# Optimization experiments

Hardware: AMD Instinct MI355X
Metric: run time of the kernel (lower is better)

## Reference

```python
import jax, jax.numpy as jnp
import numpy as np

H = 1024

def _lstm_layer(x, w_ih, w_hh, b):
    # x: [B, T, D] -> outputs [B, T, H], final (h, c) [B, H]
    B = x.shape[0]
    x_proj = jnp.einsum('btd,dg->btg', x, w_ih) + b  # [B, T, 4H]
    xp_t = jnp.swapaxes(x_proj, 0, 1)  # [T, B, 4H]

    def step(carry, xt):
        h, c = carry
        gates = xt + h @ w_hh  # [B, 4H]
        i = jax.nn.sigmoid(gates[:, :H])
        f = jax.nn.sigmoid(gates[:, H:2 * H])
        g = jnp.tanh(gates[:, 2 * H:3 * H])
        o = jax.nn.sigmoid(gates[:, 3 * H:])
        c = f * c + i * g
        h = o * jnp.tanh(c)
        return (h, c), h

    init = (jnp.zeros((B, H), x.dtype), jnp.zeros((B, H), x.dtype))
    (h_n, c_n), ys = jax.lax.scan(step, init, xp_t)
    return jnp.swapaxes(ys, 0, 1), h_n, c_n


def setup_inputs() -> dict:
    key = jax.random.key(0)
    ks = jax.random.split(key, 5)
    s = 0.1
    b = jnp.zeros((4 * H,), jnp.float32).at[H:2 * H].set(1.0)
    return {
        'x': jax.random.normal(ks[0], (32, 512, 1024), jnp.float32),
        'w_ih0': jax.random.uniform(ks[1], (1024, 4 * H), jnp.float32, -s, s),
        'w_hh0': jax.random.uniform(ks[2], (H, 4 * H), jnp.float32, -s, s),
        'b0': b,
        'w_ih1': jax.random.uniform(ks[3], (H, 4 * H), jnp.float32, -s, s),
        'w_hh1': jax.random.uniform(ks[4], (H, 4 * H), jnp.float32, -s, s),
        'b1': b,
    }


def reference(x, w_ih0, w_hh0, b0, w_ih1, w_hh1, b1):
    # Eval mode: LockedDropout / DropConnect are identity.
    y0, h0, c0 = _lstm_layer(x, w_ih0, w_hh0, b0)
    y1, h1, c1 = _lstm_layer(y0, w_ih1, w_hh1, b1)
    h_n = jnp.stack([h0, h1], axis=0)
    c_n = jnp.stack([c0, c1], axis=0)
    return y1, h_n, c_n
```

## Files before the change

kernel.cpp:

```cpp
#include <hip/hip_runtime.h>
#include <hip/hip_bf16.h>


constexpr int Hh = 1024;
constexpr int Bb = 32;
constexpr int Tt = 512;
constexpr int NWG = 256;
constexpr int NUG = 128;
constexpr int PLE  = 32 * 1024;
constexpr int ST3E = 3 * PLE;

typedef float f32x4 __attribute__((ext_vector_type(4)));
typedef int   i32x4 __attribute__((ext_vector_type(4)));

__device__ inline void mfma_bf16(f32x4& acc, i32x4 a, i32x4 b) {
    asm("s_nop 2\n\tv_mfma_f32_16x16x32_bf16 %0, %1, %2, %0"
        : "+v"(acc) : "v"(a), "v"(b));
}

__device__ inline i32x4 uload_x4(const void* p) {
    i32x4 r;
    asm volatile("global_load_dwordx4 %0, %1, off sc0 sc1\n\ts_waitcnt vmcnt(0)"
                 : "=&v"(r) : "v"(p) : "memory");
    return r;
}
__device__ inline void ustore_x4(void* p, i32x4 v) {
    asm volatile("global_store_dwordx4 %0, %1, off sc0 sc1"
                 :: "v"(p), "v"(v) : "memory");
}
__device__ inline i32x4 pload_x4(const unsigned short* p) {
    return *(const i32x4*)p;
}
__device__ inline void astore_u32(unsigned int* p, unsigned v) {
    __hip_atomic_store(p, v, __ATOMIC_RELAXED, __HIP_MEMORY_SCOPE_AGENT);
}
__device__ inline unsigned aload_u32(const unsigned int* p) {
    return __hip_atomic_load(p, __ATOMIC_RELAXED, __HIP_MEMORY_SCOPE_AGENT);
}

__device__ inline unsigned short f2bf(float f) {
    unsigned u = __float_as_uint(f);
    u += 0x7fffu + ((u >> 16) & 1u);
    return (unsigned short)(u >> 16);
}
__device__ inline float bf2f(unsigned short s) {
    return __uint_as_float((unsigned)s << 16);
}

__device__ inline float sigm(float x)  { return 1.f / (1.f + __expf(-x)); }
__device__ inline float tanh_f(float x){ return 1.f - 2.f / (__expf(2.f * x) + 1.f); }

__global__ __launch_bounds__(256) void k_xT(const float* __restrict__ x,
                                            unsigned short* __restrict__ xh,
                                            unsigned short* __restrict__ xl,
                                            int use_lo) {
    int bid = blockIdx.x;
    int t = bid >> 5, b = bid & 31;
    size_t o = ((size_t)t * Bb + b) * Hh;
    if (t == Tt) {
        ushort4 z = {0, 0, 0, 0};
        ((ushort4*)(xh + o))[threadIdx.x] = z;
        if (use_lo) ((ushort4*)(xl + o))[threadIdx.x] = z;
        return;
    }
    const float4* src = (const float4*)(x + ((size_t)b * Tt + t) * Hh);
    float4 v = src[threadIdx.x];
    ushort4 hi;
    hi.x = f2bf(v.x); hi.y = f2bf(v.y); hi.z = f2bf(v.z); hi.w = f2bf(v.w);
    ((ushort4*)(xh + o))[threadIdx.x] = hi;
    if (use_lo) {
        ushort4 lo;
        lo.x = f2bf(v.x - bf2f(hi.x));
        lo.y = f2bf(v.y - bf2f(hi.y));
        lo.z = f2bf(v.z - bf2f(hi.z));
        lo.w = f2bf(v.w - bf2f(hi.w));
        ((ushort4*)(xl + o))[threadIdx.x] = lo;
    }
}

__global__ __launch_bounds__(256) void k_warr(const float* __restrict__ w0,
                                              const float* __restrict__ w1,
                                              const float* __restrict__ w2,
                                              const float* __restrict__ w3,
                                              unsigned short* __restrict__ wh,
                                              unsigned short* __restrict__ wl,
                                              int use_lo) {
    int bid = blockIdx.x;
    int mat = bid >> 7, ug = bid & 127;
    const float* W = (mat == 0) ? w0 : (mat == 1) ? w1 : (mat == 2) ? w2 : w3;
    size_t dbase = ((size_t)(mat * NUG + ug) * 32) * Hh;
    size_t dlo   = ((size_t)(((mat >> 1) & 1) * NUG + ug) * 32) * Hh;
    const bool want_lo = use_lo && ((mat & 1) == 0);
    for (int it = 0; it < 128; ++it) {
        int idx = it * 256 + (int)threadIdx.x;
        int col = idx >> 10, k = idx & 1023;
        int cg = (col >> 3) * Hh + ug * 8 + (col & 7);
        float w = W[(size_t)k * 4096 + cg];
        unsigned short hi = f2bf(w);
        wh[dbase + (size_t)col * Hh + k] = hi;
        if (want_lo) wl[dlo + (size_t)col * Hh + k] = f2bf(w - bf2f(hi));
    }
}

template <bool USE_LO>
__global__ __launch_bounds__(512, 2) void k_lstm(
    const unsigned short* __restrict__ xTh,
    const unsigned short* __restrict__ xTl,
    const unsigned short* __restrict__ warrh,
    const unsigned short* __restrict__ warrl,
    unsigned int* __restrict__ hp0,
    unsigned int* __restrict__ hp1,
    unsigned int* __restrict__ flags,
    unsigned int* __restrict__ ectr,
    unsigned int* __restrict__ dflags,
    unsigned int* __restrict__ pfl,
    float*        __restrict__ pex,
    unsigned short* __restrict__ hstage,
    const float* __restrict__ b0,
    const float* __restrict__ b1,
    float* __restrict__ out)
{
    __shared__ float red[2][8][32][33];
    __shared__ float psum[2][32][33];
    __shared__ unsigned hsh[2][32][4];
    __shared__ int sRank;

    const int tid  = threadIdx.x;
    const int wave = tid >> 6;
    const int l    = tid & 63;
    const int wg   = blockIdx.x;
    const int kh   = wg & 1;
    const int ug   = wg >> 1;
    const int pwg  = wg ^ 1;

    unsigned xraw;
    asm volatile("s_getreg_b32 %0, hwreg(20, 0, 32)" : "=s"(xraw));
    const int xcd = (int)(xraw & 7u);
    if (tid == 0) sRank = (int)atomicAdd(&ectr[(size_t)xcd * 32], 1u);
    __syncthreads();
    const int rank = sRank;

    const int kbase = kh * 512 + ((wave + wg) & 7) * 64;

    i32x4 Bih0h[2][2], Bhh0h[2][2], Bih1h[2][2], Bhh1h[2][2];
    i32x4 Bih0l[2][2], Bih1l[2][2];
    {
        const size_t matStride = (size_t)NUG * 32 * Hh;
        const size_t wgOff = (size_t)ug * 32 * Hh;
        #pragma unroll
        for (int ch = 0; ch < 2; ++ch) {
            #pragma unroll
            for (int kk = 0; kk < 2; ++kk) {
                size_t off = (size_t)(ch * 16 + (l & 15)) * Hh
                             + kbase + kk * 32 + ((l >> 4) * 8);
                Bih0h[ch][kk] = pload_x4(warrh + 0 * matStride + wgOff + off);
                Bhh0h[ch][kk] = pload_x4(warrh + 1 * matStride + wgOff + off);
                Bih1h[ch][kk] = pload_x4(warrh + 2 * matStride + wgOff + off);
                Bhh1h[ch][kk] = pload_x4(warrh + 3 * matStride + wgOff + off);
                if (USE_LO) {
                    Bih0l[ch][kk] = pload_x4(warrl + 0 * matStride + wgOff + off);
                    Bih1l[ch][kk] = pload_x4(warrl + 1 * matStride + wgOff + off);
                }
            }
        }
        #pragma unroll
        for (int ch = 0; ch < 2; ++ch) {
            #pragma unroll
            for (int kk = 0; kk < 2; ++kk) {
                asm volatile("" : "+v"(Bih0h[ch][kk]), "+v"(Bhh0h[ch][kk]),
                                 "+v"(Bih1h[ch][kk]), "+v"(Bhh1h[ch][kk]));
                if (USE_LO)
                    asm volatile("" : "+v"(Bih0l[ch][kk]), "+v"(Bih1l[ch][kk]));
            }
        }
    }

    const int cid = tid & 127;
    const int cb  = cid & 31;
    const int ca  = (cid >> 5) & 3;
    const int a8  = kh * 4 + ca;
    const int cu  = wg * 4 + ca;
    const float* bias = (tid < 128) ? b0 : b1;
    const float bi  = bias[cu];
    const float bf_ = bias[Hh + cu];
    const float bg  = bias[2 * Hh + cu];
    const float bo  = bias[3 * Hh + cu];
    float c = 0.f;

    const int laneR = (l & 15);
    const int laneK = (l >> 4) * 8;

    f32x4 A0[2][2], A1[2][2];

    auto xterms = [&](int sidx) {
        const unsigned short* xh = xTh + (size_t)sidx * (Bb * Hh);
        const unsigned short* xl = xTl + (size_t)sidx * (Bb * Hh);
        #pragma unroll
        for (int m = 0; m < 2; ++m) {
            #pragma unroll
            for (int kk = 0; kk < 2; ++kk) {
                const size_t off = (size_t)(m * 16 + laneR) * Hh + kbase + kk * 32 + laneK;
                i32x4 axh = pload_x4(xh + off);
                i32x4 axl;
                if (USE_LO) axl = pload_x4(xl + off);
                #pragma unroll
                for (int ch = 0; ch < 2; ++ch) {
                    mfma_bf16(A0[m][ch], axh, Bih0h[ch][kk]);
                    if (USE_LO) {
                        mfma_bf16(A0[m][ch], axh, Bih0l[ch][kk]);
                        mfma_bf16(A0[m][ch], axl, Bih0h[ch][kk]);
                    }
                }
            }
        }
    };

    #pragma unroll
    for (int m = 0; m < 2; ++m)
        #pragma unroll
        for (int ch = 0; ch < 2; ++ch) A0[m][ch] = f32x4{0,0,0,0};
    xterms(0);

    unsigned nx = 0, nx32 = 0;

    for (int s = 0; s <= Tt; ++s) {
        const int par_w = s & 1;
        const int par_r = par_w ^ 1;
        const size_t parWOff32 = (size_t)par_w * (Bb * Hh);
        const size_t parROff32 = (size_t)par_r * (Bb * Hh);
        const unsigned short* stb = hstage + ((size_t)(s & 1) * 8 + xcd) * ST3E;
        const unsigned tgt = (unsigned)(s + 1);

        #pragma unroll
        for (int m = 0; m < 2; ++m)
            #pragma unroll
            for (int ch = 0; ch < 2; ++ch) A1[m][ch] = f32x4{0,0,0,0};

        #pragma unroll
        for (int m = 0; m < 2; ++m) {
            i32x4 g0h[2], g1h[2], g0l[2];
            #pragma unroll
            for (int kk = 0; kk < 2; ++kk) {
                const size_t off = (size_t)(m * 16 + laneR) * Hh + kbase + kk * 32 + laneK;
                g0h[kk] = pload_x4(stb + off);
                g1h[kk] = pload_x4(stb + 2 * PLE + off);
                if (USE_LO)
                    g0l[kk] = pload_x4(stb + PLE + off);
            }
            #pragma unroll
            for (int ch = 0; ch < 2; ++ch) {
                #pragma unroll
                for (int kk = 0; kk < 2; ++kk) {
                    mfma_bf16(A0[m][ch], g0h[kk], Bhh0h[ch][kk]);
                    mfma_bf16(A1[m][ch], g0h[kk], Bih1h[ch][kk]);
                    mfma_bf16(A1[m][ch], g1h[kk], Bhh1h[ch][kk]);
                    if (USE_LO) {
                        mfma_bf16(A0[m][ch], g0l[kk], Bhh0h[ch][kk]);
                        mfma_bf16(A1[m][ch], g0h[kk], Bih1l[ch][kk]);
                        mfma_bf16(A1[m][ch], g0l[kk], Bih1h[ch][kk]);
                    }
                }
            }
        }
        asm("s_nop 7\n\ts_nop 7"
            : "+v"(A0[0][0]), "+v"(A0[0][1]), "+v"(A0[1][0]), "+v"(A0[1][1]),
              "+v"(A1[0][0]), "+v"(A1[0][1]), "+v"(A1[1][0]), "+v"(A1[1][1]));

        {
            const int r0 = (l >> 4) * 4;
            const int cc = l & 15;
            #pragma unroll
            for (int m = 0; m < 2; ++m)
                #pragma unroll
                for (int ch = 0; ch < 2; ++ch)
                    #pragma unroll
                    for (int r = 0; r < 4; ++r) {
                        red[0][wave][m * 16 + r0 + r][ch * 16 + cc] = A0[m][ch][r];
                        red[1][wave][m * 16 + r0 + r][ch * 16 + cc] = A1[m][ch][r];
                    }
        }
        __syncthreads();

        {
            const int ly = tid >> 8, u = tid & 255;
            const int rr = u >> 3, c4 = (u & 7) * 4;
            float p0 = 0, p1 = 0, p2 = 0, p3 = 0;
            #pragma unroll
            for (int w = 0; w < 8; ++w) {
                p0 += red[ly][w][rr][c4];
                p1 += red[ly][w][rr][c4 + 1];
                p2 += red[ly][w][rr][c4 + 2];
                p3 += red[ly][w][rr][c4 + 3];
            }
            psum[ly][rr][c4] = p0;  psum[ly][rr][c4 + 1] = p1;
            psum[ly][rr][c4 + 2] = p2; psum[ly][rr][c4 + 3] = p3;
        }
        __syncthreads();

        {
            if (tid < 256) {
                const int ly = tid >> 7, u = tid & 127;
                const int rr = u >> 2, q = u & 3;
                const int pc = q * 8 + (kh ^ 1) * 4;
                i32x4 hv;
                hv[0] = __float_as_int(psum[ly][rr][pc]);
                hv[1] = __float_as_int(psum[ly][rr][pc + 1]);
                hv[2] = __float_as_int(psum[ly][rr][pc + 2]);
                hv[3] = __float_as_int(psum[ly][rr][pc + 3]);
                ustore_x4(pex + (size_t)wg * 1024 + ((ly * 32 + rr) * 4 + q) * 4, hv);
            }
            asm volatile("s_waitcnt vmcnt(0)" ::: "memory");
            __syncthreads();
            if (tid == 0) astore_u32(pfl + (size_t)wg * 32, tgt);
            if (tid == 0) {
                while (aload_u32(pfl + (size_t)pwg * 32) < tgt)
                    __builtin_amdgcn_s_sleep(1);
            }
            __syncthreads();
            if (tid < 256) {
                const int ly = tid >> 7, u = tid & 127;
                const int rr = u >> 2, q = u & 3;
                const int mc = q * 8 + kh * 4;
                i32x4 v = uload_x4(pex + (size_t)pwg * 1024 + ((ly * 32 + rr) * 4 + q) * 4);
                psum[ly][rr][mc]     += __int_as_float(v[0]);
                psum[ly][rr][mc + 1] += __int_as_float(v[1]);
                psum[ly][rr][mc + 2] += __int_as_float(v[2]);
                psum[ly][rr][mc + 3] += __int_as_float(v[3]);
            }
            __syncthreads();
        }

        if (tid < 128) {
            if (s < Tt) {
                float vi = bi  + psum[0][cb][a8];
                float vf = bf_ + psum[0][cb][8 + a8];
                float vg = bg  + psum[0][cb][16 + a8];
                float vo = bo  + psum[0][cb][24 + a8];
                float ig = sigm(vi), fg = sigm(vf), gg = tanh_f(vg), og = sigm(vo);
                c = fg * c + ig * gg;
                float h = og * tanh_f(c);
                unsigned short hh = f2bf(h);
                unsigned short hl = f2bf(h - bf2f(hh));
                hsh[0][cb][ca] = (unsigned)hh | ((unsigned)hl << 16);
                if (s == Tt - 1) {
                    out[16777216 + cb * Hh + cu] = h;
                    out[16777216 + 65536 + cb * Hh + cu] = c;
                }
            }
        } else if (tid < 256) {
            if (s >= 1) {
                const int t = s - 1;
                float vi = bi  + psum[1][cb][a8];
                float vf = bf_ + psum[1][cb][8 + a8];
                float vg = bg  + psum[1][cb][16 + a8];
                float vo = bo  + psum[1][cb][24 + a8];
                float ig = sigm(vi), fg = sigm(vf), gg = tanh_f(vg), og = sigm(vo);
                c = fg * c + ig * gg;
                float h = og * tanh_f(c);
                unsigned short hh = f2bf(h);
                hsh[1][cb][ca] = (unsigned)hh;
                out[(size_t)cb * (Tt * Hh) + (size_t)t * Hh + cu] = h;
                if (s == Tt) {
                    out[16777216 + 32768 + cb * Hh + cu] = h;
                    out[16777216 + 65536 + 32768 + cb * Hh + cu] = c;
                }
            }
        }

        if (s < Tt) {
            __syncthreads();
            if (tid < 64) {
                const int buf = tid >> 5;
                const int cbb = tid & 31;
                if (buf == 0 || s >= 1) {
                    i32x4 hv;
                    hv[0] = (int)hsh[buf][cbb][0];
                    hv[1] = (int)hsh[buf][cbb][1];
                    hv[2] = (int)hsh[buf][cbb][2];
                    hv[3] = (int)hsh[buf][cbb][3];
                    unsigned int* dst = (buf ? (hp1 + parROff32) : (hp0 + parWOff32))
                                        + (size_t)cbb * Hh + wg * 4;
                    ustore_x4(dst, hv);
                }
            }
            asm volatile("s_waitcnt vmcnt(0)" ::: "memory");
            __syncthreads();
            if (tid == 0) astore_u32(flags + (size_t)wg * 32, tgt);

            #pragma unroll
            for (int m = 0; m < 2; ++m)
                #pragma unroll
                for (int ch = 0; ch < 2; ++ch) A0[m][ch] = f32x4{0,0,0,0};
            xterms(s + 1);

            int ok = 0;
            do {
                unsigned f = (tid < 256) ? aload_u32(flags + (size_t)tid * 32) : tgt;
                ok = __syncthreads_and((int)(f >= tgt));
                if (!ok) __builtin_amdgcn_s_sleep(2);
            } while (!ok);

            if (nx == 0) {
                nx = aload_u32(ectr + (size_t)xcd * 32);
                nx32 = nx < 32u ? nx : 32u;
            }

            unsigned short* dstb = hstage + ((size_t)((s + 1) & 1) * 8 + xcd) * ST3E;
            for (int r = rank; r < 32; r += (int)nx) {
                const int buf = r >> 4;
                const unsigned int* sp = (buf == 0) ? (hp0 + parWOff32)
                                                    : (hp1 + parROff32);
                const int e = (r & 15) * 2048 + tid * 4;
                i32x4 v = uload_x4(sp + e);
                ushort4 hi4;
                hi4.x = (unsigned short)((unsigned)v[0] & 0xffffu);
                hi4.y = (unsigned short)((unsigned)v[1] & 0xffffu);
                hi4.z = (unsigned short)((unsigned)v[2] & 0xffffu);
                hi4.w = (unsigned short)((unsigned)v[3] & 0xffffu);
                unsigned short* dh = dstb + (buf == 0 ? 0 : 2 * PLE) + e;
                *(ushort4*)dh = hi4;
                if (buf == 0) {
                    ushort4 lo4;
                    lo4.x = (unsigned short)((unsigned)v[0] >> 16);
                    lo4.y = (unsigned short)((unsigned)v[1] >> 16);
                    lo4.z = (unsigned short)((unsigned)v[2] >> 16);
                    lo4.w = (unsigned short)((unsigned)v[3] >> 16);
                    *(ushort4*)(dstb + PLE + e) = lo4;
                }
            }
            asm volatile("s_waitcnt vmcnt(0)" ::: "memory");
            __syncthreads();
            if (tid == 0 && rank < 32)
                astore_u32(dflags + ((size_t)xcd * 32 + rank) * 32, tgt);
            int ok2 = 0;
            do {
                unsigned f = (tid < (int)nx32)
                    ? aload_u32(dflags + ((size_t)xcd * 32 + tid) * 32) : tgt;
                ok2 = __syncthreads_and((int)(f >= tgt));
                if (!ok2) __builtin_amdgcn_s_sleep(2);
            } while (!ok2);
        }
    }
}

extern "C" void kernel_launch(void* const* d_in, const int* in_sizes, int n_in,
                              void* d_out, int out_size, void* d_ws, size_t ws_size,
                              hipStream_t stream) {
    const float* x     = (const float*)d_in[0];
    const float* w_ih0 = (const float*)d_in[1];
    const float* w_hh0 = (const float*)d_in[2];
    const float* b0    = (const float*)d_in[3];
    const float* w_ih1 = (const float*)d_in[4];
    const float* w_hh1 = (const float*)d_in[5];
    const float* b1    = (const float*)d_in[6];
    float* out = (float*)d_out;

    const size_t SZ_WARRH = 33554432;
    const size_t SZ_WARRL = 16777216;
    const size_t SZ_XT    = 33619968;
    const size_t SZ_HP    = 262144;
    const size_t SZ_FLAGS = 32768;
    const size_t SZ_ECTR  = 1024;
    const size_t SZ_DFLG  = 32768;
    const size_t SZ_PFL   = 32768;
    const size_t SZ_PEX   = 1048576;
    const size_t SZ_STAGE = 3145728;

    char* ws = (char*)d_ws;
    unsigned short* warrh = (unsigned short*)ws;
    unsigned short* warrl = (unsigned short*)(ws + SZ_WARRH);
    unsigned short* xTh   = (unsigned short*)(ws + SZ_WARRH + SZ_WARRL);
    unsigned short* xTl   = (unsigned short*)(ws + SZ_WARRH + SZ_WARRL + SZ_XT);
    char* zbase = ws + SZ_WARRH + SZ_WARRL + 2 * SZ_XT;
    unsigned int* hp0    = (unsigned int*)zbase;
    unsigned int* hp1    = (unsigned int*)(zbase + SZ_HP);
    unsigned int* flags  = (unsigned int*)(zbase + 2 * SZ_HP);
    unsigned int* ectr   = (unsigned int*)(zbase + 2 * SZ_HP + SZ_FLAGS);
    unsigned int* dflags = (unsigned int*)(zbase + 2 * SZ_HP + SZ_FLAGS + SZ_ECTR);
    unsigned int* pfl    = (unsigned int*)(zbase + 2 * SZ_HP + SZ_FLAGS + SZ_ECTR + SZ_DFLG);
    float*        pex    = (float*)(zbase + 2 * SZ_HP + SZ_FLAGS + SZ_ECTR + SZ_DFLG + SZ_PFL);
    unsigned short* hstage =
        (unsigned short*)(zbase + 2 * SZ_HP + SZ_FLAGS + SZ_ECTR + SZ_DFLG + SZ_PFL + SZ_PEX);

    const size_t ZSZ  = 2 * SZ_HP + SZ_FLAGS + SZ_ECTR + SZ_DFLG + SZ_PFL + SZ_PEX + SZ_STAGE;
    const size_t FULL = SZ_WARRH + SZ_WARRL + 2 * SZ_XT + ZSZ;
    const bool use_lo = ws_size >= FULL;

    hipMemsetAsync(zbase, 0, ZSZ, stream);
    hipLaunchKernelGGL(k_xT,   dim3(16416), dim3(256), 0, stream, x, xTh, xTl, (int)use_lo);
    hipLaunchKernelGGL(k_warr, dim3(512),   dim3(256), 0, stream,
                       w_ih0, w_hh0, w_ih1, w_hh1, warrh, warrl, (int)use_lo);
    if (use_lo) {
        hipLaunchKernelGGL(k_lstm<true>, dim3(256), dim3(512), 0, stream,
                           xTh, xTl, warrh, warrl, hp0, hp1,
                           flags, ectr, dflags, pfl, pex, hstage, b0, b1, out);
    } else {
        hipLaunchKernelGGL(k_lstm<false>, dim3(256), dim3(512), 0, stream,
                           xTh, xTl, warrh, warrl, hp0, hp1,
                           flags, ectr, dflags, pfl, pex, hstage, b0, b1, out);
    }
}
```

Measured before the change: 5.608 ms.

## Split K across four workgroups per 16-unit group instead of two

```diff
diff --git a/kernel.cpp b/kernel.cpp
--- a/kernel.cpp
+++ b/kernel.cpp
@@ -5,8 +5,7 @@
 constexpr int Hh = 1024;
 constexpr int Bb = 32;
 constexpr int Tt = 512;
-constexpr int NWG = 256;
-constexpr int NUG = 128;
+constexpr int NUG = 64;
 constexpr int PLE  = 32 * 1024;
 constexpr int ST3E = 3 * PLE;
 
@@ -86,15 +85,15 @@
                                               unsigned short* __restrict__ wl,
                                               int use_lo) {
     int bid = blockIdx.x;
-    int mat = bid >> 7, ug = bid & 127;
+    int mat = bid >> 6, ug = bid & 63;
     const float* W = (mat == 0) ? w0 : (mat == 1) ? w1 : (mat == 2) ? w2 : w3;
-    size_t dbase = ((size_t)(mat * NUG + ug) * 32) * Hh;
-    size_t dlo   = ((size_t)(((mat >> 1) & 1) * NUG + ug) * 32) * Hh;
+    size_t dbase = ((size_t)(mat * NUG + ug) * 64) * Hh;
+    size_t dlo   = ((size_t)(((mat >> 1) & 1) * NUG + ug) * 64) * Hh;
     const bool want_lo = use_lo && ((mat & 1) == 0);
-    for (int it = 0; it < 128; ++it) {
+    for (int it = 0; it < 256; ++it) {
         int idx = it * 256 + (int)threadIdx.x;
         int col = idx >> 10, k = idx & 1023;
-        int cg = (col >> 3) * Hh + ug * 8 + (col & 7);
+        int cg = (col >> 4) * Hh + ug * 16 + (col & 15);
         float w = W[(size_t)k * 4096 + cg];
         unsigned short hi = f2bf(w);
         wh[dbase + (size_t)col * Hh + k] = hi;
@@ -120,8 +119,8 @@
     const float* __restrict__ b1,
     float* __restrict__ out)
 {
-    __shared__ float red[2][8][32][33];
-    __shared__ float psum[2][32][33];
+    __shared__ float red[2][8][32][65];
+    __shared__ float psum[2][32][65];
     __shared__ unsigned hsh[2][32][4];
     __shared__ int sRank;
 
@@ -129,9 +128,9 @@
     const int wave = tid >> 6;
     const int l    = tid & 63;
     const int wg   = blockIdx.x;
-    const int kh   = wg & 1;
-    const int ug   = wg >> 1;
-    const int pwg  = wg ^ 1;
+    const int q    = wg & 3;
+    const int qb   = wg & ~3;
+    const int ug   = wg >> 2;
 
     unsigned xraw;
     asm volatile("s_getreg_b32 %0, hwreg(20, 0, 32)" : "=s"(xraw));
@@ -140,45 +139,38 @@
     __syncthreads();
     const int rank = sRank;
 
-    const int kbase = kh * 512 + ((wave + wg) & 7) * 64;
-
-    i32x4 Bih0h[2][2], Bhh0h[2][2], Bih1h[2][2], Bhh1h[2][2];
-    i32x4 Bih0l[2][2], Bih1l[2][2];
+    const int kbase = q * 256 + ((wave + wg) & 7) * 32;
+
+    i32x4 Bih0h[4], Bhh0h[4], Bih1h[4], Bhh1h[4];
+    i32x4 Bih0l[4], Bih1l[4];
     {
-        const size_t matStride = (size_t)NUG * 32 * Hh;
-        const size_t wgOff = (size_t)ug * 32 * Hh;
-        #pragma unroll
-        for (int ch = 0; ch < 2; ++ch) {
-            #pragma unroll
-            for (int kk = 0; kk < 2; ++kk) {
-                size_t off = (size_t)(ch * 16 + (l & 15)) * Hh
-                             + kbase + kk * 32 + ((l >> 4) * 8);
-                Bih0h[ch][kk] = pload_x4(warrh + 0 * matStride + wgOff + off);
-                Bhh0h[ch][kk] = pload_x4(warrh + 1 * matStride + wgOff + off);
-                Bih1h[ch][kk] = pload_x4(warrh + 2 * matStride + wgOff + off);
-                Bhh1h[ch][kk] = pload_x4(warrh + 3 * matStride + wgOff + off);
-                if (USE_LO) {
-                    Bih0l[ch][kk] = pload_x4(warrl + 0 * matStride + wgOff + off);
-                    Bih1l[ch][kk] = pload_x4(warrl + 1 * matStride + wgOff + off);
-                }
-            }
-        }
-        #pragma unroll
-        for (int ch = 0; ch < 2; ++ch) {
-            #pragma unroll
-            for (int kk = 0; kk < 2; ++kk) {
-                asm volatile("" : "+v"(Bih0h[ch][kk]), "+v"(Bhh0h[ch][kk]),
-                                 "+v"(Bih1h[ch][kk]), "+v"(Bhh1h[ch][kk]));
-                if (USE_LO)
-                    asm volatile("" : "+v"(Bih0l[ch][kk]), "+v"(Bih1l[ch][kk]));
-            }
+        const size_t matStride = (size_t)NUG * 64 * Hh;
+        const size_t wgOff = (size_t)ug * 64 * Hh;
+        #pragma unroll
+        for (int ch = 0; ch < 4; ++ch) {
+            size_t off = (size_t)(ch * 16 + (l & 15)) * Hh + kbase + ((l >> 4) * 8);
+            Bih0h[ch] = pload_x4(warrh + 0 * matStride + wgOff + off);
+            Bhh0h[ch] = pload_x4(warrh + 1 * matStride + wgOff + off);
+            Bih1h[ch] = pload_x4(warrh + 2 * matStride + wgOff + off);
+            Bhh1h[ch] = pload_x4(warrh + 3 * matStride + wgOff + off);
+            if (USE_LO) {
+                Bih0l[ch] = pload_x4(warrl + 0 * matStride + wgOff + off);
+                Bih1l[ch] = pload_x4(warrl + 1 * matStride + wgOff + off);
+            }
+        }
+        #pragma unroll
+        for (int ch = 0; ch < 4; ++ch) {
+            asm volatile("" : "+v"(Bih0h[ch]), "+v"(Bhh0h[ch]),
+                             "+v"(Bih1h[ch]), "+v"(Bhh1h[ch]));
+            if (USE_LO)
+                asm volatile("" : "+v"(Bih0l[ch]), "+v"(Bih1l[ch]));
         }
     }
 
     const int cid = tid & 127;
     const int cb  = cid & 31;
     const int ca  = (cid >> 5) & 3;
-    const int a8  = kh * 4 + ca;
+    const int a16 = q * 4 + ca;
     const int cu  = wg * 4 + ca;
     const float* bias = (tid < 128) ? b0 : b1;
     const float bi  = bias[cu];
@@ -190,26 +182,23 @@
     const int laneR = (l & 15);
     const int laneK = (l >> 4) * 8;
 
-    f32x4 A0[2][2], A1[2][2];
+    f32x4 A0[2][4], A1[2][4];
 
     auto xterms = [&](int sidx) {
         const unsigned short* xh = xTh + (size_t)sidx * (Bb * Hh);
         const unsigned short* xl = xTl + (size_t)sidx * (Bb * Hh);
         #pragma unroll
         for (int m = 0; m < 2; ++m) {
-            #pragma unroll
-            for (int kk = 0; kk < 2; ++kk) {
-                const size_t off = (size_t)(m * 16 + laneR) * Hh + kbase + kk * 32 + laneK;
-                i32x4 axh = pload_x4(xh + off);
-                i32x4 axl;
-                if (USE_LO) axl = pload_x4(xl + off);
-                #pragma unroll
-                for (int ch = 0; ch < 2; ++ch) {
-                    mfma_bf16(A0[m][ch], axh, Bih0h[ch][kk]);
-                    if (USE_LO) {
-                        mfma_bf16(A0[m][ch], axh, Bih0l[ch][kk]);
-                        mfma_bf16(A0[m][ch], axl, Bih0h[ch][kk]);
-                    }
+            const size_t off = (size_t)(m * 16 + laneR) * Hh + kbase + laneK;
+            i32x4 axh = pload_x4(xh + off);
+            i32x4 axl;
+            if (USE_LO) axl = pload_x4(xl + off);
+            #pragma unroll
+            for (int ch = 0; ch < 4; ++ch) {
+                mfma_bf16(A0[m][ch], axh, Bih0h[ch]);
+                if (USE_LO) {
+                    mfma_bf16(A0[m][ch], axh, Bih0l[ch]);
+                    mfma_bf16(A0[m][ch], axl, Bih0h[ch]);
                 }
             }
         }
@@ -218,7 +207,7 @@
     #pragma unroll
     for (int m = 0; m < 2; ++m)
         #pragma unroll
-        for (int ch = 0; ch < 2; ++ch) A0[m][ch] = f32x4{0,0,0,0};
+        for (int ch = 0; ch < 4; ++ch) A0[m][ch] = f32x4{0,0,0,0};
     xterms(0);
 
     unsigned nx = 0, nx32 = 0;
@@ -234,37 +223,32 @@
         #pragma unroll
         for (int m = 0; m < 2; ++m)
             #pragma unroll
-            for (int ch = 0; ch < 2; ++ch) A1[m][ch] = f32x4{0,0,0,0};
+            for (int ch = 0; ch < 4; ++ch) A1[m][ch] = f32x4{0,0,0,0};
 
         #pragma unroll
         for (int m = 0; m < 2; ++m) {
-            i32x4 g0h[2], g1h[2], g0l[2];
-            #pragma unroll
-            for (int kk = 0; kk < 2; ++kk) {
-                const size_t off = (size_t)(m * 16 + laneR) * Hh + kbase + kk * 32 + laneK;
-                g0h[kk] = pload_x4(stb + off);
-                g1h[kk] = pload_x4(stb + 2 * PLE + off);
-                if (USE_LO)
-                    g0l[kk] = pload_x4(stb + PLE + off);
-            }
-            #pragma unroll
-            for (int ch = 0; ch < 2; ++ch) {
-                #pragma unroll
-                for (int kk = 0; kk < 2; ++kk) {
-                    mfma_bf16(A0[m][ch], g0h[kk], Bhh0h[ch][kk]);
-                    mfma_bf16(A1[m][ch], g0h[kk], Bih1h[ch][kk]);
-                    mfma_bf16(A1[m][ch], g1h[kk], Bhh1h[ch][kk]);
-                    if (USE_LO) {
-                        mfma_bf16(A0[m][ch], g0l[kk], Bhh0h[ch][kk]);
-                        mfma_bf16(A1[m][ch], g0h[kk], Bih1l[ch][kk]);
-                        mfma_bf16(A1[m][ch], g0l[kk], Bih1h[ch][kk]);
-                    }
+            const size_t off = (size_t)(m * 16 + laneR) * Hh + kbase + laneK;
+            i32x4 g0h = pload_x4(stb + off);
+            i32x4 g1h = pload_x4(stb + 2 * PLE + off);
+            i32x4 g0l;
+            if (USE_LO) g0l = pload_x4(stb + PLE + off);
+            #pragma unroll
+            for (int ch = 0; ch < 4; ++ch) {
+                mfma_bf16(A0[m][ch], g0h, Bhh0h[ch]);
+                mfma_bf16(A1[m][ch], g0h, Bih1h[ch]);
+                mfma_bf16(A1[m][ch], g1h, Bhh1h[ch]);
+                if (USE_LO) {
+                    mfma_bf16(A0[m][ch], g0l, Bhh0h[ch]);
+                    mfma_bf16(A1[m][ch], g0h, Bih1l[ch]);
+                    mfma_bf16(A1[m][ch], g0l, Bih1h[ch]);
                 }
             }
         }
         asm("s_nop 7\n\ts_nop 7"
-            : "+v"(A0[0][0]), "+v"(A0[0][1]), "+v"(A0[1][0]), "+v"(A0[1][1]),
-              "+v"(A1[0][0]), "+v"(A1[0][1]), "+v"(A1[1][0]), "+v"(A1[1][1]));
+            : "+v"(A0[0][0]), "+v"(A0[0][1]), "+v"(A0[0][2]), "+v"(A0[0][3]),
+              "+v"(A0[1][0]), "+v"(A0[1][1]), "+v"(A0[1][2]), "+v"(A0[1][3]),
+              "+v"(A1[0][0]), "+v"(A1[0][1]), "+v"(A1[0][2]), "+v"(A1[0][3]),
+              "+v"(A1[1][0]), "+v"(A1[1][1]), "+v"(A1[1][2]), "+v"(A1[1][3]));
 
         {
             const int r0 = (l >> 4) * 4;
@@ -272,7 +256,7 @@
             #pragma unroll
             for (int m = 0; m < 2; ++m)
                 #pragma unroll
-                for (int ch = 0; ch < 2; ++ch)
+                for (int ch = 0; ch < 4; ++ch)
                     #pragma unroll
                     for (int r = 0; r < 4; ++r) {
                         red[0][wave][m * 16 + r0 + r][ch * 16 + cc] = A0[m][ch][r];
@@ -283,59 +267,69 @@
 
         {
             const int ly = tid >> 8, u = tid & 255;
-            const int rr = u >> 3, c4 = (u & 7) * 4;
-            float p0 = 0, p1 = 0, p2 = 0, p3 = 0;
-            #pragma unroll
-            for (int w = 0; w < 8; ++w) {
-                p0 += red[ly][w][rr][c4];
-                p1 += red[ly][w][rr][c4 + 1];
-                p2 += red[ly][w][rr][c4 + 2];
-                p3 += red[ly][w][rr][c4 + 3];
-            }
-            psum[ly][rr][c4] = p0;  psum[ly][rr][c4 + 1] = p1;
-            psum[ly][rr][c4 + 2] = p2; psum[ly][rr][c4 + 3] = p3;
+            const int rr = u >> 3, c8 = (u & 7) * 8;
+            float p[8];
+            #pragma unroll
+            for (int j = 0; j < 8; ++j) p[j] = 0.f;
+            #pragma unroll
+            for (int w = 0; w < 8; ++w)
+                #pragma unroll
+                for (int j = 0; j < 8; ++j) p[j] += red[ly][w][rr][c8 + j];
+            #pragma unroll
+            for (int j = 0; j < 8; ++j) psum[ly][rr][c8 + j] = p[j];
         }
         __syncthreads();
 
         {
-            if (tid < 256) {
-                const int ly = tid >> 7, u = tid & 127;
-                const int rr = u >> 2, q = u & 3;
-                const int pc = q * 8 + (kh ^ 1) * 4;
-                i32x4 hv;
-                hv[0] = __float_as_int(psum[ly][rr][pc]);
-                hv[1] = __float_as_int(psum[ly][rr][pc + 1]);
-                hv[2] = __float_as_int(psum[ly][rr][pc + 2]);
-                hv[3] = __float_as_int(psum[ly][rr][pc + 3]);
-                ustore_x4(pex + (size_t)wg * 1024 + ((ly * 32 + rr) * 4 + q) * 4, hv);
-            }
+            const int ly = tid >> 8, u = tid & 255;
+            const int rr = u >> 3, c8 = (u & 7) * 8;
+            float* base = pex + (size_t)wg * 4096 + ((size_t)ly * 32 + rr) * 64 + c8;
+            i32x4 v0, v1;
+            v0[0] = __float_as_int(psum[ly][rr][c8]);
+            v0[1] = __float_as_int(psum[ly][rr][c8 + 1]);
+            v0[2] = __float_as_int(psum[ly][rr][c8 + 2]);
+            v0[3] = __float_as_int(psum[ly][rr][c8 + 3]);
+            v1[0] = __float_as_int(psum[ly][rr][c8 + 4]);
+            v1[1] = __float_as_int(psum[ly][rr][c8 + 5]);
+            v1[2] = __float_as_int(psum[ly][rr][c8 + 6]);
+            v1[3] = __float_as_int(psum[ly][rr][c8 + 7]);
+            ustore_x4(base, v0);
+            ustore_x4(base + 4, v1);
             asm volatile("s_waitcnt vmcnt(0)" ::: "memory");
             __syncthreads();
             if (tid == 0) astore_u32(pfl + (size_t)wg * 32, tgt);
-            if (tid == 0) {
-                while (aload_u32(pfl + (size_t)pwg * 32) < tgt)
-                    __builtin_amdgcn_s_sleep(1);
-            }
-            __syncthreads();
+            int okp = 0;
+            do {
+                unsigned f = tgt;
+                if (tid < 4 && tid != q)
+                    f = aload_u32(pfl + (size_t)(qb + tid) * 32);
+                okp = __syncthreads_and((int)(f >= tgt));
+                if (!okp) __builtin_amdgcn_s_sleep(1);
+            } while (!okp);
             if (tid < 256) {
-                const int ly = tid >> 7, u = tid & 127;
-                const int rr = u >> 2, q = u & 3;
-                const int mc = q * 8 + kh * 4;
-                i32x4 v = uload_x4(pex + (size_t)pwg * 1024 + ((ly * 32 + rr) * 4 + q) * 4);
-                psum[ly][rr][mc]     += __int_as_float(v[0]);
-                psum[ly][rr][mc + 1] += __int_as_float(v[1]);
-                psum[ly][rr][mc + 2] += __int_as_float(v[2]);
-                psum[ly][rr][mc + 3] += __int_as_float(v[3]);
+                const int ly2 = tid >> 7, u2 = tid & 127;
+                const int rr2 = u2 >> 2, g = u2 & 3;
+                const int col = g * 16 + q * 4;
+                #pragma unroll
+                for (int pp = 0; pp < 4; ++pp) {
+                    if (pp == q) continue;
+                    i32x4 v = uload_x4(pex + (size_t)(qb + pp) * 4096
+                                       + ((size_t)ly2 * 32 + rr2) * 64 + col);
+                    psum[ly2][rr2][col]     += __int_as_float(v[0]);
+                    psum[ly2][rr2][col + 1] += __int_as_float(v[1]);
+                    psum[ly2][rr2][col + 2] += __int_as_float(v[2]);
+                    psum[ly2][rr2][col + 3] += __int_as_float(v[3]);
+                }
             }
             __syncthreads();
         }
 
         if (tid < 128) {
             if (s < Tt) {
-                float vi = bi  + psum[0][cb][a8];
-                float vf = bf_ + psum[0][cb][8 + a8];
-                float vg = bg  + psum[0][cb][16 + a8];
-                float vo = bo  + psum[0][cb][24 + a8];
+                float vi = bi  + psum[0][cb][a16];
+                float vf = bf_ + psum[0][cb][16 + a16];
+                float vg = bg  + psum[0][cb][32 + a16];
+                float vo = bo  + psum[0][cb][48 + a16];
                 float ig = sigm(vi), fg = sigm(vf), gg = tanh_f(vg), og = sigm(vo);
                 c = fg * c + ig * gg;
                 float h = og * tanh_f(c);
@@ -350,10 +344,10 @@
         } else if (tid < 256) {
             if (s >= 1) {
                 const int t = s - 1;
-                float vi = bi  + psum[1][cb][a8];
-                float vf = bf_ + psum[1][cb][8 + a8];
-                float vg = bg  + psum[1][cb][16 + a8];
-                float vo = bo  + psum[1][cb][24 + a8];
+                float vi = bi  + psum[1][cb][a16];
+                float vf = bf_ + psum[1][cb][16 + a16];
+                float vg = bg  + psum[1][cb][32 + a16];
+                float vo = bo  + psum[1][cb][48 + a16];
                 float ig = sigm(vi), fg = sigm(vf), gg = tanh_f(vg), og = sigm(vo);
                 c = fg * c + ig * gg;
                 float h = og * tanh_f(c);
@@ -390,7 +384,7 @@
             #pragma unroll
             for (int m = 0; m < 2; ++m)
                 #pragma unroll
-                for (int ch = 0; ch < 2; ++ch) A0[m][ch] = f32x4{0,0,0,0};
+                for (int ch = 0; ch < 4; ++ch) A0[m][ch] = f32x4{0,0,0,0};
             xterms(s + 1);
 
             int ok = 0;
@@ -463,7 +457,7 @@
     const size_t SZ_ECTR  = 1024;
     const size_t SZ_DFLG  = 32768;
     const size_t SZ_PFL   = 32768;
-    const size_t SZ_PEX   = 1048576;
+    const size_t SZ_PEX   = 4194304;
     const size_t SZ_STAGE = 3145728;
 
     char* ws = (char*)d_ws;
@@ -488,7 +482,7 @@
 
     hipMemsetAsync(zbase, 0, ZSZ, stream);
     hipLaunchKernelGGL(k_xT,   dim3(16416), dim3(256), 0, stream, x, xTh, xTl, (int)use_lo);
-    hipLaunchKernelGGL(k_warr, dim3(512),   dim3(256), 0, stream,
+    hipLaunchKernelGGL(k_warr, dim3(256),   dim3(256), 0, stream,
                        w_ih0, w_hh0, w_ih1, w_hh1, warrh, warrl, (int)use_lo);
     if (use_lo) {
         hipLaunchKernelGGL(k_lstm<true>, dim3(256), dim3(512), 0, stream,
```

After: 6.821 ms. 21.6% more time.
